# Optimization experiments

Measured on AMD Instinct MI355X. Metric: run time of the kernel, lower is better.

## Reference

```python
import jax, jax.numpy as jnp
import numpy as np

B, L, H = 2, 2048, 2048
NH, KVH = 16, 4
D = H // NH          # 128
G = NH // KVH        # 4 query heads per kv head
LN_EPS = 1e-12


def setup_inputs() -> dict:
    key = jax.random.key(0)
    ks = jax.random.split(key, 6)
    s = 0.02
    return {
        "hidden_state": jax.random.normal(ks[0], (B, L, H), jnp.float32),
        "mask": jnp.zeros((B, 1, 1, L), jnp.float32),
        "Wq": jax.random.normal(ks[1], (H, H), jnp.float32) * s,
        "bq": jnp.zeros((H,), jnp.float32),
        "Wk": jax.random.normal(ks[2], (KVH * D, H), jnp.float32) * s,
        "bk": jnp.zeros((KVH * D,), jnp.float32),
        "Wv": jax.random.normal(ks[3], (KVH * D, H), jnp.float32) * s,
        "bv": jnp.zeros((KVH * D,), jnp.float32),
        "Wo": jax.random.normal(ks[4], (H, H), jnp.float32) * s,
        "bo": jnp.zeros((H,), jnp.float32),
        "ln_g": jnp.ones((H,), jnp.float32),
        "ln_b": jnp.zeros((H,), jnp.float32),
    }


def _layernorm(x, g, b):
    mu = jnp.mean(x, axis=-1, keepdims=True)
    var = jnp.mean(jnp.square(x - mu), axis=-1, keepdims=True)
    return (x - mu) * jax.lax.rsqrt(var + LN_EPS) * g + b


def reference(hidden_state, mask, Wq, bq, Wk, bk, Wv, bv, Wo, bo, ln_g, ln_b):
    x = hidden_state
    # projections: b l (h d)
    q = x @ Wq.T + bq            # [B,L,NH*D]
    k = x @ Wk.T + bk            # [B,L,KVH*D]
    v = x @ Wv.T + bv            # [B,L,KVH*D]
    # b l (h d) -> b h l d, with q heads grouped per kv head (GQA broadcast,
    # mathematically identical to repeat_kv + dense SDPA)
    q = q.reshape(B, L, KVH, G, D).transpose(0, 2, 3, 1, 4)   # [B,KVH,G,L,D]
    k = k.reshape(B, L, KVH, D).transpose(0, 2, 1, 3)         # [B,KVH,L,D]
    v = v.reshape(B, L, KVH, D).transpose(0, 2, 1, 3)         # [B,KVH,L,D]
    scale = 1.0 / jnp.sqrt(jnp.float32(D))
    scores = jnp.einsum('bkgld,bkmd->bkglm', q, k) * scale    # [B,KVH,G,L,L]
    scores = scores + mask[:, :, None]                         # broadcast [B,1,1,1,L]
    attn = jax.nn.softmax(scores, axis=-1)
    out = jnp.einsum('bkglm,bkmd->bkgld', attn, v)            # [B,KVH,G,L,D]
    out = out.transpose(0, 3, 1, 2, 4).reshape(B, L, H)       # b h l d -> b l (h d)
    # SelfOutput: dense + residual + layernorm
    out = out @ Wo.T + bo
    return _layernorm(out + x, ln_g, ln_b)
```

## Files before the change

kernel.cpp:

```cpp
#include <hip/hip_runtime.h>
#include <math.h>

typedef short v8s __attribute__((ext_vector_type(8)));
typedef short v4s __attribute__((ext_vector_type(4)));
typedef float v4f __attribute__((ext_vector_type(4)));
typedef unsigned long long ull;

constexpr int L_ = 2048;
constexpr int H_ = 2048;
constexpr float LOG2E = 1.4426950408889634f;
constexpr float QSCALE = 0.08838834764831845f * LOG2E;

__device__ inline unsigned short f2bf(float f) {
    unsigned int u = __float_as_uint(f);
    u += 0x7fffu + ((u >> 16) & 1u);
    return (unsigned short)(u >> 16);
}

__device__ inline unsigned int pk2bf(float lo, float hi) {
    unsigned int a = __float_as_uint(lo) + 0x8000u;
    unsigned int b = __float_as_uint(hi) + 0x8000u;
    return __builtin_amdgcn_perm(b, a, 0x07060302);
}

__device__ inline void async16(const void* g, void* l) {
    __builtin_amdgcn_global_load_lds(
        (const __attribute__((address_space(1))) unsigned int*)g,
        (__attribute__((address_space(3))) unsigned int*)l, 16, 0, 0);
}

__global__ __launch_bounds__(256) void conv_all(
    const float* __restrict__ x,  const float* __restrict__ wq,
    const float* __restrict__ wk, const float* __restrict__ wv,
    const float* __restrict__ wo, const float* __restrict__ mask,
    unsigned short* __restrict__ xb, unsigned short* __restrict__ wqkvb,
    unsigned short* __restrict__ wob, float* __restrict__ maskL)
{
    int u = blockIdx.x * 256 + threadIdx.x;
    const float* s;
    unsigned short* d;
    if (u < 1048576)      { s = x  + (size_t)u * 8;             d = xb   + (size_t)u * 8; }
    else if (u < 1572864) { size_t t = (size_t)(u - 1048576) * 8; s = wq + t; d = wqkvb + t; }
    else if (u < 1703936) { size_t t = (size_t)(u - 1572864) * 8; s = wk + t; d = wqkvb + (size_t)2048 * 2048 + t; }
    else if (u < 1835008) { size_t t = (size_t)(u - 1703936) * 8; s = wv + t; d = wqkvb + (size_t)2560 * 2048 + t; }
    else if (u < 2359296) { size_t t = (size_t)(u - 1835008) * 8; s = wo + t; d = wob + t; }
    else if (u < 2359808) {
        int m = (u - 2359296) * 8;
        float4 a = *(const float4*)(mask + m);
        float4 b = *(const float4*)(mask + m + 4);
        float4 oa = {a.x * LOG2E, a.y * LOG2E, a.z * LOG2E, a.w * LOG2E};
        float4 ob = {b.x * LOG2E, b.y * LOG2E, b.z * LOG2E, b.w * LOG2E};
        *(float4*)(maskL + m) = oa;
        *(float4*)(maskL + m + 4) = ob;
        return;
    } else return;
    float4 a = *(const float4*)s;
    float4 b = *(const float4*)(s + 4);
    v8s o;
    o[0] = (short)f2bf(a.x); o[1] = (short)f2bf(a.y);
    o[2] = (short)f2bf(a.z); o[3] = (short)f2bf(a.w);
    o[4] = (short)f2bf(b.x); o[5] = (short)f2bf(b.y);
    o[6] = (short)f2bf(b.z); o[7] = (short)f2bf(b.w);
    *(v8s*)d = o;
}

template <int MODE>
__global__ __launch_bounds__(256) void gemm_mfma(
    const unsigned short* __restrict__ A, const unsigned short* __restrict__ W,
    const float* __restrict__ b0, const float* __restrict__ b1,
    const float* __restrict__ b2,
    unsigned short* __restrict__ oq, unsigned short* __restrict__ ok,
    unsigned short* __restrict__ ov,
    float* __restrict__ of, const float* __restrict__ resid,
    int K, int N)
{
    __shared__ short SM[3 * 8192];

    const int tid  = threadIdx.x;
    const int lane = tid & 63;
    const int wave = tid >> 6;
    const int lid  = lane & 15;
    const int g    = lane >> 4;
    const int wr   = wave >> 1, wc = wave & 1;
    const int row0 = blockIdx.y * 128, col0 = blockIdx.x * 128;

    auto stage = [&](int k0, int buf) {
#pragma unroll
        for (int i = 0; i < 2; ++i) {
            int idx = tid + i * 256;
            int r = idx >> 2, s = idx & 3;
            int c = s ^ ((r >> 1) & 3);
            async16(A + (size_t)(row0 + r) * K + k0 + c * 8,
                    &SM[buf * 8192 + idx * 8]);
            async16(W + (size_t)(col0 + r) * K + k0 + c * 8,
                    &SM[buf * 8192 + 4096 + idx * 8]);
        }
    };

    v4f acc[4][4];
#pragma unroll
    for (int i = 0; i < 4; ++i)
#pragma unroll
        for (int j = 0; j < 4; ++j) acc[i][j] = (v4f){0.f, 0.f, 0.f, 0.f};

    stage(0, 0);
    stage(32, 1);
    int p = 0;
    for (int k0 = 0; k0 < K; k0 += 32) {
        __syncthreads();
        if (k0 + 64 < K) {
            int nb = p + 2; if (nb >= 3) nb -= 3;
            stage(k0 + 64, nb);
        }
        const short* As = &SM[p * 8192];
        const short* Bs = &SM[p * 8192 + 4096];

        v8s af[4], bf[4];
#pragma unroll
        for (int t = 0; t < 4; ++t) {
            int ra = wr * 64 + t * 16 + lid;
            int rb = wc * 64 + t * 16 + lid;
            af[t] = *(const v8s*)&As[ra * 32 + ((g ^ ((ra >> 1) & 3)) * 8)];
            bf[t] = *(const v8s*)&Bs[rb * 32 + ((g ^ ((rb >> 1) & 3)) * 8)];
        }
#pragma unroll
        for (int mt = 0; mt < 4; ++mt)
#pragma unroll
            for (int nt = 0; nt < 4; ++nt)
                acc[mt][nt] = __builtin_amdgcn_mfma_f32_16x16x32_bf16(
                    af[mt], bf[nt], acc[mt][nt], 0, 0, 0);
        if (++p == 3) p = 0;
    }

    const int crow = row0 + wr * 64, ccol = col0 + wc * 64;
    if (MODE == 0) {
#pragma unroll
        for (int mt = 0; mt < 4; ++mt)
#pragma unroll
            for (int nt = 0; nt < 4; ++nt) {
                int cc = ccol + nt * 16 + lid;
                float bb = b0[cc];
#pragma unroll
                for (int r = 0; r < 4; ++r) {
                    int rr = crow + mt * 16 + g * 4 + r;
                    of[(size_t)rr * N + cc] =
                        acc[mt][nt][r] + bb + resid[(size_t)rr * N + cc];
                }
            }
    } else {
        const int seg = (col0 < 2048) ? 0 : (col0 < 2560 ? 1 : 2);
#pragma unroll
        for (int mt = 0; mt < 4; ++mt)
#pragma unroll
            for (int nt = 0; nt < 4; ++nt) {
                int cc = ccol + nt * 16 + lid;
                if (seg == 0) {
                    float bb = b0[cc];
#pragma unroll
                    for (int r = 0; r < 4; ++r) {
                        int rr = crow + mt * 16 + g * 4 + r;
                        oq[(size_t)rr * 2048 + cc] =
                            f2bf((acc[mt][nt][r] + bb) * QSCALE);
                    }
                } else if (seg == 1) {
                    float bb = b1[cc - 2048];
#pragma unroll
                    for (int r = 0; r < 4; ++r) {
                        int rr = crow + mt * 16 + g * 4 + r;
                        ok[(size_t)rr * 512 + (cc - 2048)] =
                            f2bf(acc[mt][nt][r] + bb);
                    }
                } else {
                    float bb = b2[cc - 2560];
                    int dprime = cc - 2560;
                    int colb = (crow & 2047) + ((mt >> 1) << 5) +
                               (g << 3) + ((mt & 1) << 2);
                    size_t vrow = (size_t)((crow >> 11) * 512 + dprime);
                    unsigned int lo =
                        (unsigned int)f2bf(acc[mt][nt][0] + bb) |
                        ((unsigned int)f2bf(acc[mt][nt][1] + bb) << 16);
                    unsigned int hi =
                        (unsigned int)f2bf(acc[mt][nt][2] + bb) |
                        ((unsigned int)f2bf(acc[mt][nt][3] + bb) << 16);
                    uint2 pkv; pkv.x = lo; pkv.y = hi;
                    *(uint2*)&ov[vrow * 2048 + colb] = pkv;
                }
            }
    }
}

__global__ __launch_bounds__(512) void flash_mfma(
    const unsigned short* __restrict__ Q,
    const unsigned short* __restrict__ K,
    const unsigned short* __restrict__ Vt,
    const float* __restrict__ maskL,
    unsigned short* __restrict__ AO)
{
    __shared__ short K_s[2][32 * 128];
    __shared__ short V_s[3][128 * 32];

    const int tid  = threadIdx.x;
    const int lane = tid & 63;
    const int wave = tid >> 6;
    const int lid  = lane & 15;
    const int g    = lane >> 4;
    const int lh   = (lid >> 2) & 3;

    const int c7   = blockIdx.x & 7;
    const int kvh  = c7 >> 1;
    const int b    = c7 & 1;
    const int rest = blockIdx.x >> 3;
    const int h    = kvh * 4 + (rest & 3);
    const int q0   = (rest >> 2) * 256;
    const int wq   = wave * 32;

    const float* mb = maskL + b * L_;

    const unsigned short* pK;
    const unsigned short* pV;
    {
        int kr = tid >> 4, ks = tid & 15;
        pK = K + ((size_t)(b * L_ + kr)) * 512 + kvh * 128 +
             ((ks ^ (kr & 15)) * 8);
        int vd = tid >> 2, vs = tid & 3;
        pV = Vt + ((size_t)(b * 512 + kvh * 128 + vd)) * 2048 +
             ((vs ^ ((vd >> 2) & 3)) * 8);
    }

    v8s bq[2][4];
    {
        const size_t base = ((size_t)(b * L_ + q0 + wq + lid)) * 2048 + h * 128;
#pragma unroll
        for (int qt = 0; qt < 2; ++qt)
#pragma unroll
            for (int kc = 0; kc < 4; ++kc)
                bq[qt][kc] = *(const v8s*)(Q + base + (size_t)qt * 16 * 2048 +
                                           kc * 32 + g * 8);
    }

    v4f oacc[2][8];
#pragma unroll
    for (int mt = 0; mt < 2; ++mt)
#pragma unroll
        for (int nt = 0; nt < 8; ++nt) oacc[mt][nt] = (v4f){0.f, 0.f, 0.f, 0.f};
    float lsm[2] = {0.f, 0.f};
    v4f sacc[2][2];
    v8s ap[2];

    auto qk = [&](int k0, const short* Ks) {
#pragma unroll
        for (int kt = 0; kt < 2; ++kt) {
            float4 mk = *(const float4*)&mb[k0 + kt * 16 + g * 4];
            v4f seed = {mk.x, mk.y, mk.z, mk.w};
            sacc[kt][0] = seed;
            sacc[kt][1] = seed;
        }
#pragma unroll
        for (int kc = 0; kc < 4; ++kc)
#pragma unroll
            for (int kt = 0; kt < 2; ++kt) {
                v8s ak = *(const v8s*)&Ks[(kt * 16 + lid) * 128 +
                                          (((kc * 4 + g) ^ lid) * 8)];
#pragma unroll
                for (int qt = 0; qt < 2; ++qt)
                    sacc[kt][qt] = __builtin_amdgcn_mfma_f32_16x16x32_bf16(
                        ak, bq[qt][kc], sacc[kt][qt], 0, 0, 0);
            }
    };

    auto pv = [&](const short* Vs) {
#pragma unroll
        for (int nt = 0; nt < 8; ++nt) {
            v8s bv = *(const v8s*)&Vs[(nt * 16 + lid) * 32 + ((g ^ lh) * 8)];
#pragma unroll
            for (int mt = 0; mt < 2; ++mt)
                oacc[mt][nt] = __builtin_amdgcn_mfma_f32_16x16x32_bf16(
                    ap[mt], bv, oacc[mt][nt], 0, 0, 0);
        }
    };

    auto sm = [&]() {
#pragma unroll
        for (int qt = 0; qt < 2; ++qt) {
            float e0 = __builtin_amdgcn_exp2f(sacc[0][qt][0]);
            float e1 = __builtin_amdgcn_exp2f(sacc[0][qt][1]);
            float e2 = __builtin_amdgcn_exp2f(sacc[0][qt][2]);
            float e3 = __builtin_amdgcn_exp2f(sacc[0][qt][3]);
            float f0 = __builtin_amdgcn_exp2f(sacc[1][qt][0]);
            float f1 = __builtin_amdgcn_exp2f(sacc[1][qt][1]);
            float f2 = __builtin_amdgcn_exp2f(sacc[1][qt][2]);
            float f3 = __builtin_amdgcn_exp2f(sacc[1][qt][3]);
            lsm[qt] += ((e0 + e1) + (e2 + e3)) + ((f0 + f1) + (f2 + f3));
            union { uint4 u; v8s v; } pa;
            pa.u.x = pk2bf(e0, e1);
            pa.u.y = pk2bf(e2, e3);
            pa.u.z = pk2bf(f0, f1);
            pa.u.w = pk2bf(f2, f3);
            ap[qt] = pa.v;
        }
    };

    async16(pK, &K_s[0][tid * 8]);
    async16(pV, &V_s[0][tid * 8]);
    __syncthreads();
    pK += 32 * 512; pV += 32;
    async16(pK, &K_s[1][tid * 8]);
    async16(pV, &V_s[1][tid * 8]);
    qk(0, K_s[0]);
    sm();

    int vprev = 0;
    for (int t = 1; t < 64; ++t) {
        __syncthreads();
        if (t + 1 < 64) {
            pK += 32 * 512; pV += 32;
            async16(pK, &K_s[(t + 1) & 1][tid * 8]);
            async16(pV, &V_s[(t + 1) % 3][tid * 8]);
        }
        qk(t * 32, K_s[t & 1]);
        pv(V_s[vprev]);
        sm();
        if (++vprev == 3) vprev = 0;
    }
    pv(V_s[0]);

#pragma unroll
    for (int qt = 0; qt < 2; ++qt) {
        lsm[qt] += __shfl_xor(lsm[qt], 16);
        lsm[qt] += __shfl_xor(lsm[qt], 32);
    }
#pragma unroll
    for (int mt = 0; mt < 2; ++mt) {
        float linv[4];
#pragma unroll
        for (int r = 0; r < 4; ++r) linv[r] = 1.0f / __shfl(lsm[mt], g * 4 + r);
#pragma unroll
        for (int nt = 0; nt < 8; ++nt)
#pragma unroll
            for (int r = 0; r < 4; ++r) {
                size_t orow = (size_t)(b * L_ + q0 + wq + mt * 16 + g * 4 + r);
                AO[orow * 2048 + h * 128 + nt * 16 + lid] =
                    f2bf(oacc[mt][nt][r] * linv[r]);
            }
    }
}

__global__ __launch_bounds__(256) void ln_kernel(
    const float* __restrict__ P, const float* __restrict__ g,
    const float* __restrict__ bta, float* __restrict__ Out)
{
    const int row = blockIdx.x;
    const int tid = threadIdx.x;
    const float* p = P + (size_t)row * H_;

    float vals[8];
    float s = 0.f;
#pragma unroll
    for (int it = 0; it < 2; ++it) {
        int c = tid * 4 + it * 1024;
        float4 a = *(const float4*)&p[c];
        vals[it * 4 + 0] = a.x; vals[it * 4 + 1] = a.y;
        vals[it * 4 + 2] = a.z; vals[it * 4 + 3] = a.w;
        s += a.x + a.y + a.z + a.w;
    }
    __shared__ float red[4];
    float t = s;
#pragma unroll
    for (int off = 32; off > 0; off >>= 1) t += __shfl_xor(t, off);
    if ((tid & 63) == 0) red[tid >> 6] = t;
    __syncthreads();
    float mean = (red[0] + red[1] + red[2] + red[3]) * (1.f / (float)H_);

    float vsum = 0.f;
#pragma unroll
    for (int i = 0; i < 8; ++i) {
        float d = vals[i] - mean;
        vsum += d * d;
    }
    __syncthreads();
    t = vsum;
#pragma unroll
    for (int off = 32; off > 0; off >>= 1) t += __shfl_xor(t, off);
    if ((tid & 63) == 0) red[tid >> 6] = t;
    __syncthreads();
    float var = (red[0] + red[1] + red[2] + red[3]) * (1.f / (float)H_);
    float rs  = 1.f / sqrtf(var + 1e-12f);

#pragma unroll
    for (int it = 0; it < 2; ++it) {
        int c = tid * 4 + it * 1024;
        float4 gv = *(const float4*)&g[c];
        float4 bv = *(const float4*)&bta[c];
        float4 ov;
        ov.x = (vals[it * 4 + 0] - mean) * rs * gv.x + bv.x;
        ov.y = (vals[it * 4 + 1] - mean) * rs * gv.y + bv.y;
        ov.z = (vals[it * 4 + 2] - mean) * rs * gv.z + bv.z;
        ov.w = (vals[it * 4 + 3] - mean) * rs * gv.w + bv.w;
        *(float4*)&Out[(size_t)row * H_ + c] = ov;
    }
}

extern "C" void kernel_launch(void* const* d_in, const int* in_sizes, int n_in,
                              void* d_out, int out_size, void* d_ws, size_t ws_size,
                              hipStream_t stream)
{
    const float* x    = (const float*)d_in[0];
    const float* mask = (const float*)d_in[1];
    const float* Wq   = (const float*)d_in[2];
    const float* bq   = (const float*)d_in[3];
    const float* Wk   = (const float*)d_in[4];
    const float* bk   = (const float*)d_in[5];
    const float* Wv   = (const float*)d_in[6];
    const float* bv   = (const float*)d_in[7];
    const float* Wo   = (const float*)d_in[8];
    const float* bo   = (const float*)d_in[9];
    const float* lng  = (const float*)d_in[10];
    const float* lnb  = (const float*)d_in[11];
    float* out = (float*)d_out;

    char* ws = (char*)d_ws;
    unsigned short* xb    = (unsigned short*)(ws);
    unsigned short* wqkv  = (unsigned short*)(ws + 16777216);
    float*          maskL = (float*)         (ws + 29360128);
    unsigned short* q     = (unsigned short*)(ws + 29376512);
    unsigned short* k     = (unsigned short*)(ws + 46153728);
    unsigned short* vt    = (unsigned short*)(ws + 54542336);
    unsigned short* ao    = (unsigned short*)(ws + 58736640);
    unsigned short* wob   = (unsigned short*)(ws + 75513856);
    float*          pj    = (float*)(ws);

    dim3 blk(256);
    conv_all<<<9218, blk, 0, stream>>>(x, Wq, Wk, Wv, Wo, mask,
                                       xb, wqkv, wob, maskL);

    gemm_mfma<3><<<dim3(24, 32), blk, 0, stream>>>(
        xb, wqkv, bq, bk, bv, q, k, vt, nullptr, nullptr, 2048, 3072);

    flash_mfma<<<dim3(256), dim3(512), 0, stream>>>(q, k, vt, maskL, ao);

    gemm_mfma<0><<<dim3(16, 32), blk, 0, stream>>>(
        ao, wob, bo, nullptr, nullptr, nullptr, nullptr, nullptr, pj, x, 2048, 2048);
    ln_kernel<<<4096, blk, 0, stream>>>(pj, lng, lnb, out);
}
```

Baseline: 344.8 us.

## Stagger softmax and PV MFMA order across waves with ping-pong P buffers

Double-buffers the softmax probability fragments (even/odd) so that within an iteration, half the waves run the PV MFMAs before computing softmax and the other half compute softmax first. Sched barriers enforce this order, so MFMA-heavy and exp/VALU-heavy phases from different waves can overlap on the same SIMD. It also raises wave priority around the MFMA blocks and precomputes the LDS offsets for K and V. The cost is more registers for the second P buffer and the offset arrays, plus divergent code paths per wave group.

After: 352.5 us. +2.2%, slower.

```diff
diff --git a/kernel.cpp b/kernel.cpp
--- a/kernel.cpp
+++ b/kernel.cpp
@@ -227,6 +227,17 @@
              ((vs ^ ((vd >> 2) & 3)) * 8);
     }
 
+    int koff[2][4];
+#pragma unroll
+    for (int kt = 0; kt < 2; ++kt)
+#pragma unroll
+        for (int kc = 0; kc < 4; ++kc)
+            koff[kt][kc] = (kt * 16 + lid) * 128 + (((kc * 4 + g) ^ lid) * 8);
+    int voff[8];
+#pragma unroll
+    for (int nt = 0; nt < 8; ++nt)
+        voff[nt] = (nt * 16 + lid) * 32 + ((g ^ lh) * 8);
+
     v8s bq[2][4];
     {
         const size_t base = ((size_t)(b * L_ + q0 + wq + lid)) * 2048 + h * 128;
@@ -245,7 +256,9 @@
         for (int nt = 0; nt < 8; ++nt) oacc[mt][nt] = (v4f){0.f, 0.f, 0.f, 0.f};
     float lsm[2] = {0.f, 0.f};
     v4f sacc[2][2];
-    v8s ap[2];
+
+    struct P2 { v8s a0, a1; };
+    P2 apE, apO;
 
     auto qk = [&](int k0, const short* Ks) {
 #pragma unroll
@@ -255,49 +268,70 @@
             sacc[kt][0] = seed;
             sacc[kt][1] = seed;
         }
+        __builtin_amdgcn_s_setprio(1);
 #pragma unroll
         for (int kc = 0; kc < 4; ++kc)
 #pragma unroll
             for (int kt = 0; kt < 2; ++kt) {
-                v8s ak = *(const v8s*)&Ks[(kt * 16 + lid) * 128 +
-                                          (((kc * 4 + g) ^ lid) * 8)];
-#pragma unroll
-                for (int qt = 0; qt < 2; ++qt)
-                    sacc[kt][qt] = __builtin_amdgcn_mfma_f32_16x16x32_bf16(
-                        ak, bq[qt][kc], sacc[kt][qt], 0, 0, 0);
+                v8s ak = *(const v8s*)&Ks[koff[kt][kc]];
+                sacc[kt][0] = __builtin_amdgcn_mfma_f32_16x16x32_bf16(
+                    ak, bq[0][kc], sacc[kt][0], 0, 0, 0);
+                sacc[kt][1] = __builtin_amdgcn_mfma_f32_16x16x32_bf16(
+                    ak, bq[1][kc], sacc[kt][1], 0, 0, 0);
             }
+        __builtin_amdgcn_s_setprio(0);
     };
 
-    auto pv = [&](const short* Vs) {
+    auto pvf = [&](const P2& app, const short* Vs) {
+        __builtin_amdgcn_s_setprio(1);
 #pragma unroll
         for (int nt = 0; nt < 8; ++nt) {
-            v8s bv = *(const v8s*)&Vs[(nt * 16 + lid) * 32 + ((g ^ lh) * 8)];
-#pragma unroll
-            for (int mt = 0; mt < 2; ++mt)
-                oacc[mt][nt] = __builtin_amdgcn_mfma_f32_16x16x32_bf16(
-                    ap[mt], bv, oacc[mt][nt], 0, 0, 0);
-        }
+            v8s bv = *(const v8s*)&Vs[voff[nt]];
+            oacc[0][nt] = __builtin_amdgcn_mfma_f32_16x16x32_bf16(
+                app.a0, bv, oacc[0][nt], 0, 0, 0);
+            oacc[1][nt] = __builtin_amdgcn_mfma_f32_16x16x32_bf16(
+                app.a1, bv, oacc[1][nt], 0, 0, 0);
+        }
+        __builtin_amdgcn_s_setprio(0);
     };
 
-    auto sm = [&]() {
-#pragma unroll
-        for (int qt = 0; qt < 2; ++qt) {
-            float e0 = __builtin_amdgcn_exp2f(sacc[0][qt][0]);
-            float e1 = __builtin_amdgcn_exp2f(sacc[0][qt][1]);
-            float e2 = __builtin_amdgcn_exp2f(sacc[0][qt][2]);
-            float e3 = __builtin_amdgcn_exp2f(sacc[0][qt][3]);
-            float f0 = __builtin_amdgcn_exp2f(sacc[1][qt][0]);
-            float f1 = __builtin_amdgcn_exp2f(sacc[1][qt][1]);
-            float f2 = __builtin_amdgcn_exp2f(sacc[1][qt][2]);
-            float f3 = __builtin_amdgcn_exp2f(sacc[1][qt][3]);
-            lsm[qt] += ((e0 + e1) + (e2 + e3)) + ((f0 + f1) + (f2 + f3));
+    auto sm = [&]() -> P2 {
+        P2 r;
+        {
+            float e0 = __builtin_amdgcn_exp2f(sacc[0][0][0]);
+            float e1 = __builtin_amdgcn_exp2f(sacc[0][0][1]);
+            float e2 = __builtin_amdgcn_exp2f(sacc[0][0][2]);
+            float e3 = __builtin_amdgcn_exp2f(sacc[0][0][3]);
+            float f0 = __builtin_amdgcn_exp2f(sacc[1][0][0]);
+            float f1 = __builtin_amdgcn_exp2f(sacc[1][0][1]);
+            float f2 = __builtin_amdgcn_exp2f(sacc[1][0][2]);
+            float f3 = __builtin_amdgcn_exp2f(sacc[1][0][3]);
+            lsm[0] += ((e0 + e1) + (e2 + e3)) + ((f0 + f1) + (f2 + f3));
             union { uint4 u; v8s v; } pa;
             pa.u.x = pk2bf(e0, e1);
             pa.u.y = pk2bf(e2, e3);
             pa.u.z = pk2bf(f0, f1);
             pa.u.w = pk2bf(f2, f3);
-            ap[qt] = pa.v;
-        }
+            r.a0 = pa.v;
+        }
+        {
+            float e0 = __builtin_amdgcn_exp2f(sacc[0][1][0]);
+            float e1 = __builtin_amdgcn_exp2f(sacc[0][1][1]);
+            float e2 = __builtin_amdgcn_exp2f(sacc[0][1][2]);
+            float e3 = __builtin_amdgcn_exp2f(sacc[0][1][3]);
+            float f0 = __builtin_amdgcn_exp2f(sacc[1][1][0]);
+            float f1 = __builtin_amdgcn_exp2f(sacc[1][1][1]);
+            float f2 = __builtin_amdgcn_exp2f(sacc[1][1][2]);
+            float f3 = __builtin_amdgcn_exp2f(sacc[1][1][3]);
+            lsm[1] += ((e0 + e1) + (e2 + e3)) + ((f0 + f1) + (f2 + f3));
+            union { uint4 u; v8s v; } pa;
+            pa.u.x = pk2bf(e0, e1);
+            pa.u.y = pk2bf(e2, e3);
+            pa.u.z = pk2bf(f0, f1);
+            pa.u.w = pk2bf(f2, f3);
+            r.a1 = pa.v;
+        }
+        return r;
     };
 
     async16(pK, &K_s[0][tid * 8]);
@@ -307,8 +341,9 @@
     async16(pK, &K_s[1][tid * 8]);
     async16(pV, &V_s[1][tid * 8]);
     qk(0, K_s[0]);
-    sm();
-
+    apE = sm();
+
+    const bool early = (wave < 4);
     int vprev = 0;
     for (int t = 1; t < 64; ++t) {
         __syncthreads();
@@ -317,12 +352,33 @@
             async16(pK, &K_s[(t + 1) & 1][tid * 8]);
             async16(pV, &V_s[(t + 1) % 3][tid * 8]);
         }
-        qk(t * 32, K_s[t & 1]);
-        pv(V_s[vprev]);
-        sm();
+        const short* Ks  = K_s[t & 1];
+        const short* Vsp = V_s[vprev];
+        qk(t * 32, Ks);
+        if (t & 1) {
+            if (early) {
+                pvf(apE, Vsp);
+                __builtin_amdgcn_sched_barrier(0);
+                apO = sm();
+            } else {
+                apO = sm();
+                __builtin_amdgcn_sched_barrier(0);
+                pvf(apE, Vsp);
+            }
+        } else {
+            if (early) {
+                pvf(apO, Vsp);
+                __builtin_amdgcn_sched_barrier(0);
+                apE = sm();
+            } else {
+                apE = sm();
+                __builtin_amdgcn_sched_barrier(0);
+                pvf(apO, Vsp);
+            }
+        }
         if (++vprev == 3) vprev = 0;
     }
-    pv(V_s[0]);
+    pvf(apO, V_s[0]);
 
 #pragma unroll
     for (int qt = 0; qt < 2; ++qt) {
```
